# Kernel tuning notes

Measured on AMD Instinct MI355X. Metric: run time of the kernel, lower is better.

Reference implementation:

```python
import jax, jax.numpy as jnp
import numpy as np


def _conv(x, w):
    # 'same'-padded NCHW conv, stride 1, no bias (matches nn.Conv2d(..., padding=k//2, bias=False))
    return jax.lax.conv_general_dilated(x, w, (1, 1), 'SAME',
                                        dimension_numbers=('NCHW', 'OIHW', 'NCHW'))


def setup_inputs() -> dict:
    key = jax.random.key(0)
    ks = jax.random.split(key, 11)
    b, C, H, W = 8, 64, 192, 192
    n_classes, n_space = 2, 8
    return {
        'x': jax.random.normal(ks[0], (b, C, H, W), jnp.float32),
        'class_score': jax.random.normal(ks[1], (b, n_classes, H, W), jnp.float32),
        # to_cspace: Conv2d(1, n_space-1, 3, padding=1)
        'W_cspace': jax.random.normal(ks[2], (n_space - 1, 1, 3, 3), jnp.float32) * 0.1,
        # to_xspace: Conv2d(C, C*n_space, 3, padding=1)
        'W_xspace': jax.random.normal(ks[3], (C * n_space, C, 3, 3), jnp.float32) * 0.02,
        # 1x1 convs stored as squeezed vectors (no bias)
        'W_combine_space': jax.random.normal(ks[4], (n_space,), jnp.float32) * 0.3,  # Conv2d(n_space,1,1)
        'W_cvalue': jax.random.normal(ks[5], (n_space,), jnp.float32) * 0.3,        # Conv2d(1,n_space,1)
        'W_attn': jax.random.normal(ks[6], (n_space,), jnp.float32) * 0.3,          # Conv2d(1,n_space,1)
        'W_combine': jax.random.normal(ks[7], (n_space,), jnp.float32) * 0.3,       # Conv2d(n_space,1,1)
        # single_conv: Conv2d(C,C,3) + BatchNorm2d(C) + ReLU
        'W_single': jax.random.normal(ks[8], (C, C, 3, 3), jnp.float32) * 0.02,
        'bn_gamma': jnp.ones((C,), jnp.float32),
        'bn_beta': jnp.zeros((C,), jnp.float32),
    }


def reference(x, class_score, W_cspace, W_xspace, W_combine_space, W_cvalue,
              W_attn, W_combine, W_single, bn_gamma, bn_beta):
    b, C, H, Wd = x.shape
    nc = class_score.shape[1]           # n_classes
    s = W_cvalue.shape[0]               # n_space
    class_prob = jax.nn.sigmoid(class_score)                       # (b, c, H, W)

    # per-class spatial 'spaces'
    space0 = class_prob.reshape(b * nc, 1, H, Wd)                  # (b*c, 1, H, W)
    space = jnp.concatenate([space0, jax.nn.sigmoid(_conv(space0, W_cspace))], axis=1)  # (b*c, s, H, W)
    space_norm = space / jnp.sum(space, axis=(2, 3), keepdims=True)
    space_norm = space_norm.reshape(b, nc, s, H, Wd).transpose(0, 2, 1, 3, 4)  # (b, s, c, H, W)

    # project x into s spaces, then contract over spatial dims (replaces broadcast-mul + double sum)
    xv = _conv(x, W_xspace).reshape(b, s, C, H, Wd)                # (b, s, d, H, W)
    tok = jnp.einsum('bsdhw,bschw->bscd', xv, space_norm)          # (b, s, c, d)
    tok = jnp.einsum('s,bscd->bcd', W_combine_space, tok)          # combine_space 1x1 conv -> (b, c, d)

    # class value / attention (1x1 convs over a singleton channel == broadcast scale)
    cval = tok[:, None] * W_cvalue[None, :, None, None]            # (b, s, c, d)
    attn = class_prob.reshape(b, nc, H * Wd).transpose(0, 2, 1)    # (b, hw, c)
    attn = jax.nn.sigmoid(attn[:, None] * W_attn[None, :, None, None])  # (b, s, hw, c)

    # attention matmul + combine 1x1 conv fused into one contraction (linear ops commute)
    info = jnp.einsum('s,bsnc,bscd->bnd', W_combine, attn, cval)   # (b, hw, d)
    info = info.transpose(0, 2, 1).reshape(b, C, H, Wd)            # (b, d, H, W)

    # single_conv: conv3x3 -> BatchNorm2d (training-mode batch stats, biased var) -> ReLU
    y = _conv(info, W_single)
    mean = jnp.mean(y, axis=(0, 2, 3), keepdims=True)
    var = jnp.var(y, axis=(0, 2, 3), keepdims=True)
    y = jax.nn.relu((y - mean) * jax.lax.rsqrt(var + 1e-5)
                    * bn_gamma[None, :, None, None] + bn_beta[None, :, None, None])
    return x + y
```

## Files before the change

### kernel.cpp

```cpp
#include <hip/hip_runtime.h>
#include <math.h>

#define B   8
#define C   64
#define HH  192
#define WWD 192
#define P   (HH*WWD)
#define NC  2
#define NS  8
#define PP  (194*194)

#define OFF_SPACE 0
#define OFF_WT    0
#define OFF_GM    294912
#define OFF_WST   884736
#define OFF_SPART 4817408
#define OFF_R     4835840
#define OFF_TOK2  4909568
#define OFF_U     4910592
#define OFF_STP   4919808
#define OFF_SCALE 4956672
#define OFF_SHIFT 4956736
#define WS_FLOATS 4956800

__device__ __forceinline__ float sigm(float x) { return 1.0f / (1.0f + expf(-x)); }

__global__ void k_space(const float* __restrict__ cs, const float* __restrict__ Wc,
                        float* __restrict__ spp, float* __restrict__ Spart) {
    int m = blockIdx.y;
    int bx = blockIdx.x;
    int p = bx * 256 + threadIdx.x;
    int h = p / WWD, w = p - (p / WWD) * WWD;
    float cp[9];
    #pragma unroll
    for (int ky = 0; ky < 3; ky++)
        #pragma unroll
        for (int kx = 0; kx < 3; kx++) {
            int hh = h + ky - 1, ww = w + kx - 1;
            float v = 0.f;
            if ((unsigned)hh < HH && (unsigned)ww < WWD)
                v = sigm(cs[m * P + hh * WWD + ww]);
            cp[ky * 3 + kx] = v;
        }
    float ch[8];
    ch[0] = cp[4];
    #pragma unroll
    for (int j = 0; j < 7; j++) {
        float a = 0.f;
        #pragma unroll
        for (int k = 0; k < 9; k++) a += Wc[j * 9 + k] * cp[k];
        ch[j + 1] = sigm(a);
    }
    #pragma unroll
    for (int q = 0; q < 8; q++)
        spp[(m * 8 + q) * PP + (h + 1) * 194 + (w + 1)] = ch[q];
    __shared__ float red[4][8];
    int lane = threadIdx.x & 63, wave = threadIdx.x >> 6;
    #pragma unroll
    for (int q = 0; q < 8; q++) {
        float v = ch[q];
        for (int off = 32; off > 0; off >>= 1) v += __shfl_down(v, off);
        if (lane == 0) red[wave][q] = v;
    }
    __syncthreads();
    if (threadIdx.x < 8) {
        int q = threadIdx.x;
        Spart[(m * 8 + q) * 144 + bx] = red[0][q] + red[1][q] + red[2][q] + red[3][q];
    }
}

__launch_bounds__(256, 3)
__global__ void k_R2(const float* __restrict__ x, const float* __restrict__ spp,
                     float* __restrict__ R) {
    int ig = blockIdx.x;
    int scz = blockIdx.y;
    int b  = blockIdx.z;
    int sc = scz & 15;
    int half = scz >> 4;
    int s = sc >> 1, c = sc & 1;
    const float* xb = x + (b * C + ig * 8) * P;
    const float* sp = spp + ((b * NC + c) * NS + s) * PP;

    float acc[8][9];
    #pragma unroll
    for (int i = 0; i < 8; i++)
        #pragma unroll
        for (int t = 0; t < 9; t++) acc[i][t] = 0.f;

    for (int it = half * 18; it < half * 18 + 18; it++) {
        int p0 = it * 1024 + threadIdx.x * 4;
        int h = p0 / WWD, w0 = p0 - (p0 / WWD) * WWD;
        float4 xv[8];
        #pragma unroll
        for (int i = 0; i < 8; i++) xv[i] = *(const float4*)(xb + i * P + p0);
        float g[3][6];
        #pragma unroll
        for (int ty = 0; ty < 3; ty++) {
            const float* rp = sp + (h + 2 - ty) * 194 + w0;
            float4 ga; float2 gb;
            __builtin_memcpy(&ga, rp, 16);
            __builtin_memcpy(&gb, rp + 4, 8);
            g[ty][0] = ga.x; g[ty][1] = ga.y; g[ty][2] = ga.z;
            g[ty][3] = ga.w; g[ty][4] = gb.x; g[ty][5] = gb.y;
        }
        #pragma unroll
        for (int ty = 0; ty < 3; ty++)
            #pragma unroll
            for (int tx = 0; tx < 3; tx++) {
                float g0 = g[ty][2 - tx], g1 = g[ty][3 - tx];
                float g2 = g[ty][4 - tx], g3 = g[ty][5 - tx];
                #pragma unroll
                for (int i = 0; i < 8; i++) {
                    float a = acc[i][ty * 3 + tx];
                    a += xv[i].x * g0; a += xv[i].y * g1;
                    a += xv[i].z * g2; a += xv[i].w * g3;
                    acc[i][ty * 3 + tx] = a;
                }
            }
    }

    __shared__ float red[4][72];
    int lane = threadIdx.x & 63, wave = threadIdx.x >> 6;
    #pragma unroll
    for (int i = 0; i < 8; i++)
        #pragma unroll
        for (int t = 0; t < 9; t++) {
            float v = acc[i][t];
            for (int off = 32; off > 0; off >>= 1) v += __shfl_down(v, off);
            if (lane == 0) red[wave][i * 9 + t] = v;
        }
    __syncthreads();
    if (threadIdx.x < 72) {
        int i = threadIdx.x / 9, t = threadIdx.x - (threadIdx.x / 9) * 9;
        float v = red[0][threadIdx.x] + red[1][threadIdx.x] +
                  red[2][threadIdx.x] + red[3][threadIdx.x];
        atomicAdd(&R[((b * 16 + sc) * 64 + (ig * 8 + i)) * 9 + t], v);
    }
}

__global__ void k_wtb(const float* __restrict__ Wxs, const float* __restrict__ Ws,
                      float* __restrict__ Wt, float* __restrict__ WsT) {
    int blk = blockIdx.x;
    if (blk < 1152) {
        int o = blk * 256 + threadIdx.x;
        int d = o & 63, r = o >> 6;
        int s = r / 576, t = r - s * 576;
        Wt[o] = Wxs[(s * 64 + d) * 576 + t];
    } else {
        int o = (blk - 1152) * 256 + threadIdx.x;
        int ci = o / 576, q = o - ci * 576;
        int t = q >> 6, oc = q & 63;
        WsT[o] = Ws[(oc * 64 + ci) * 9 + t];
    }
}

__global__ void k_g(const float* __restrict__ cs, const float* __restrict__ Wcval,
                    const float* __restrict__ Wattn, const float* __restrict__ Wcomb,
                    float* __restrict__ gmap) {
    int m = blockIdx.y;
    int p = blockIdx.x * 256 + threadIdx.x;
    float wa[8], wt[8];
    #pragma unroll
    for (int s = 0; s < 8; s++) { wa[s] = Wcomb[s] * Wcval[s]; wt[s] = Wattn[s]; }
    float cp = sigm(cs[m * P + p]);
    float a = 0.f;
    #pragma unroll
    for (int s = 0; s < 8; s++) a += wa[s] * sigm(cp * wt[s]);
    gmap[m * P + p] = a;
}

__global__ void k_tok2(const float* __restrict__ Wt, const float* __restrict__ Wcs,
                       const float* __restrict__ R, const float* __restrict__ Spart,
                       float* __restrict__ tok2) {
    int bc = blockIdx.x, s = blockIdx.y, tz = blockIdx.z;
    int d = threadIdx.x;
    const float* spp = Spart + (bc * 8 + s) * 144;
    float sv = 0.f;
    for (int k = d; k < 144; k += 64) sv += spp[k];
    #pragma unroll
    for (int msk = 32; msk >= 1; msk >>= 1) sv += __shfl_xor(sv, msk);

    const float* Rp = R + ((bc & 1) + ((bc >> 1) * 16 + s * 2)) * 576;
    const float* Wp = Wt + s * 576 * 64 + d;
    float a = 0.f;
    int t0 = tz * 144;
    #pragma unroll 8
    for (int t = t0; t < t0 + 144; t++) a += Wp[t * 64] * Rp[t];
    float val = a * Wcs[s] / sv;
    atomicAdd(&tok2[bc * C + d], val);
}

__global__ void k_U(const float* __restrict__ WsT, const float* __restrict__ tok2,
                    float* __restrict__ U) {
    int b = blockIdx.x, m = blockIdx.y;
    int tid = threadIdx.x;
    int oc = tid & 63, t = tid >> 6;
    __shared__ float tok[64];
    if (tid < 64) tok[tid] = tok2[(b * NC + m) * C + tid];
    __syncthreads();
    float a = 0.f;
    #pragma unroll 8
    for (int ci = 0; ci < C; ci++) a += WsT[ci * 576 + tid] * tok[ci];
    U[((b * C + oc) * 2 + m) * 9 + t] = a;
}

__device__ __forceinline__ void stage_g(const float* __restrict__ gmap, int b, int ty0, int tx0,
                                        float* h0, float* h1) {
    const float* g0p = gmap + (b * NC + 0) * P;
    const float* g1p = gmap + (b * NC + 1) * P;
    for (int idx = threadIdx.x; idx < 34 * 34; idx += 256) {
        int i = idx / 34, j = idx - (idx / 34) * 34;
        int gy = ty0 - 1 + i, gx = tx0 - 1 + j;
        float a0 = 0.f, a1 = 0.f;
        if ((unsigned)gy < HH && (unsigned)gx < WWD) {
            int p = gy * WWD + gx;
            a0 = g0p[p]; a1 = g1p[p];
        }
        h0[i * 35 + j] = a0; h1[i * 35 + j] = a1;
    }
}

__launch_bounds__(256)
__global__ void k_cs(const float* __restrict__ gmap, const float* __restrict__ U,
                     float* __restrict__ STp) {
    int tile = blockIdx.x, og2 = blockIdx.y, b = blockIdx.z;
    int ty0 = (tile / 6) * 32, tx0 = (tile % 6) * 32;
    __shared__ float h0[34 * 35], h1[34 * 35];
    stage_g(gmap, b, ty0, tx0, h0, h1);
    __syncthreads();

    int w = __builtin_amdgcn_readfirstlane(threadIdx.x >> 6);
    int lane = threadIdx.x & 63;
    for (int g4 = 0; g4 < 4; g4++) {
        int oc0 = (og2 * 4 + g4) * 8 + w * 2;
        float u0[2][9], u1[2][9];
        #pragma unroll
        for (int j = 0; j < 2; j++) {
            const float* up = U + ((b * C + oc0 + j) * 2) * 9;
            #pragma unroll
            for (int t = 0; t < 9; t++) { u0[j][t] = up[t]; u1[j][t] = up[9 + t]; }
        }
        float s1[2] = {0.f, 0.f}, s2[2] = {0.f, 0.f};
        for (int it = 0; it < 4; it++) {
            int row = it * 8 + (lane >> 3);
            int c0 = (lane & 7) * 4;
            float g0v[3][6], g1v[3][6];
            #pragma unroll
            for (int dy = 0; dy < 3; dy++)
                #pragma unroll
                for (int dx = 0; dx < 6; dx++) {
                    g0v[dy][dx] = h0[(row + dy) * 35 + c0 + dx];
                    g1v[dy][dx] = h1[(row + dy) * 35 + c0 + dx];
                }
            #pragma unroll
            for (int j = 0; j < 2; j++)
                #pragma unroll
                for (int px = 0; px < 4; px++) {
                    float y = 0.f;
                    #pragma unroll
                    for (int ky = 0; ky < 3; ky++)
                        #pragma unroll
                        for (int kx = 0; kx < 3; kx++) {
                            y += u0[j][ky * 3 + kx] * g0v[ky][px + kx];
                            y += u1[j][ky * 3 + kx] * g1v[ky][px + kx];
                        }
                    s1[j] += y; s2[j] += y * y;
                }
        }
        #pragma unroll
        for (int j = 0; j < 2; j++) {
            float a = s1[j], q = s2[j];
            for (int off = 32; off > 0; off >>= 1) { a += __shfl_down(a, off); q += __shfl_down(q, off); }
            if (lane == 0) {
                int slot = b * 36 + tile;
                STp[slot * 64 + (oc0 + j)] = a;
                STp[288 * 64 + slot * 64 + (oc0 + j)] = q;
            }
        }
    }
}

__global__ void k_bnfin(const float* __restrict__ STp, const float* __restrict__ gamma,
                        const float* __restrict__ beta, float* __restrict__ scale,
                        float* __restrict__ shift) {
    int oc = threadIdx.x & 63, q = threadIdx.x >> 6;
    double s = 0.0, s2 = 0.0;
    for (int k = q * 72; k < q * 72 + 72; k++) {
        s  += (double)STp[k * 64 + oc];
        s2 += (double)STp[288 * 64 + k * 64 + oc];
    }
    __shared__ double ls[4][64], ls2[4][64];
    ls[q][oc] = s; ls2[q][oc] = s2;
    __syncthreads();
    if (threadIdx.x < 64) {
        double S  = ls[0][oc] + ls[1][oc] + ls[2][oc] + ls[3][oc];
        double S2 = ls2[0][oc] + ls2[1][oc] + ls2[2][oc] + ls2[3][oc];
        double n = (double)(B * P);
        double mean = S / n;
        double var = S2 / n - mean * mean;
        float sc = gamma[oc] * rsqrtf((float)var + 1e-5f);
        scale[oc] = sc;
        shift[oc] = beta[oc] - (float)mean * sc;
    }
}

__launch_bounds__(256)
__global__ void k_fin2(const float* __restrict__ gmap, const float* __restrict__ U,
                       const float* __restrict__ x,
                       const float* __restrict__ scale, const float* __restrict__ shift,
                       float* __restrict__ out) {
    int tile = blockIdx.x, og2 = blockIdx.y, b = blockIdx.z;
    int ty0 = (tile / 6) * 32, tx0 = (tile % 6) * 32;
    __shared__ float h0[34 * 35], h1[34 * 35];
    stage_g(gmap, b, ty0, tx0, h0, h1);
    __syncthreads();

    int w = __builtin_amdgcn_readfirstlane(threadIdx.x >> 6);
    int lane = threadIdx.x & 63;
    for (int g4 = 0; g4 < 4; g4++) {
        int oc0 = (og2 * 4 + g4) * 8 + w * 2;
        float u0[2][9], u1[2][9], sc[2], sh[2];
        #pragma unroll
        for (int j = 0; j < 2; j++) {
            const float* up = U + ((b * C + oc0 + j) * 2) * 9;
            #pragma unroll
            for (int t = 0; t < 9; t++) { u0[j][t] = up[t]; u1[j][t] = up[9 + t]; }
            sc[j] = scale[oc0 + j]; sh[j] = shift[oc0 + j];
        }
        for (int it = 0; it < 4; it++) {
            int row = it * 8 + (lane >> 3);
            int c0 = (lane & 7) * 4;
            float g0v[3][6], g1v[3][6];
            #pragma unroll
            for (int dy = 0; dy < 3; dy++)
                #pragma unroll
                for (int dx = 0; dx < 6; dx++) {
                    g0v[dy][dx] = h0[(row + dy) * 35 + c0 + dx];
                    g1v[dy][dx] = h1[(row + dy) * 35 + c0 + dx];
                }
            #pragma unroll
            for (int j = 0; j < 2; j++) {
                float y4[4];
                #pragma unroll
                for (int px = 0; px < 4; px++) {
                    float y = 0.f;
                    #pragma unroll
                    for (int ky = 0; ky < 3; ky++)
                        #pragma unroll
                        for (int kx = 0; kx < 3; kx++) {
                            y += u0[j][ky * 3 + kx] * g0v[ky][px + kx];
                            y += u1[j][ky * 3 + kx] * g1v[ky][px + kx];
                        }
                    y4[px] = y;
                }
                int ga = (b * C + oc0 + j) * P + (ty0 + row) * WWD + tx0 + c0;
                float4 xv = *(const float4*)(x + ga);
                float4 ov;
                ov.x = fmaxf(y4[0] * sc[j] + sh[j], 0.f) + xv.x;
                ov.y = fmaxf(y4[1] * sc[j] + sh[j], 0.f) + xv.y;
                ov.z = fmaxf(y4[2] * sc[j] + sh[j], 0.f) + xv.z;
                ov.w = fmaxf(y4[3] * sc[j] + sh[j], 0.f) + xv.w;
                *(float4*)(out + ga) = ov;
            }
        }
    }
}

extern "C" void kernel_launch(void* const* d_in, const int* in_sizes, int n_in,
                              void* d_out, int out_size, void* d_ws, size_t ws_size,
                              hipStream_t stream) {
    const float* x     = (const float*)d_in[0];
    const float* cs    = (const float*)d_in[1];
    const float* Wc    = (const float*)d_in[2];
    const float* Wxs   = (const float*)d_in[3];
    const float* Wcsp  = (const float*)d_in[4];
    const float* Wcval = (const float*)d_in[5];
    const float* Wattn = (const float*)d_in[6];
    const float* Wcomb = (const float*)d_in[7];
    const float* Wsing = (const float*)d_in[8];
    const float* gamma = (const float*)d_in[9];
    const float* beta  = (const float*)d_in[10];
    float* ws  = (float*)d_ws;
    float* out = (float*)d_out;

    float* spp   = ws + OFF_SPACE;
    float* Wt    = ws + OFF_WT;
    float* gmap  = ws + OFF_GM;
    float* WsT   = ws + OFF_WST;
    float* Spart = ws + OFF_SPART;
    float* R     = ws + OFF_R;
    float* tok2  = ws + OFF_TOK2;
    float* U     = ws + OFF_U;
    float* STp   = ws + OFF_STP;
    float* scale = ws + OFF_SCALE;
    float* shift = ws + OFF_SHIFT;

    hipMemsetAsync(ws, 0, (size_t)(OFF_TOK2 + 1024) * sizeof(float), stream);

    k_space<<<dim3(144, 16), 256, 0, stream>>>(cs, Wc, spp, Spart);
    k_R2   <<<dim3(8, 32, 8), 256, 0, stream>>>(x, spp, R);
    k_wtb  <<<dim3(1296), 256, 0, stream>>>(Wxs, Wsing, Wt, WsT);
    k_g    <<<dim3(144, 16), 256, 0, stream>>>(cs, Wcval, Wattn, Wcomb, gmap);
    k_tok2 <<<dim3(16, 8, 4), 64, 0, stream>>>(Wt, Wcsp, R, Spart, tok2);
    k_U    <<<dim3(8, 2), 576, 0, stream>>>(WsT, tok2, U);
    k_cs   <<<dim3(36, 2, 8), 256, 0, stream>>>(gmap, U, STp);
    k_bnfin<<<1, 256, 0, stream>>>(STp, gamma, beta, scale, shift);
    k_fin2 <<<dim3(36, 2, 8), 256, 0, stream>>>(gmap, U, x, scale, shift, out);
}
```

Baseline: 380.2 us.

## Compute spatial correlation R with split-bf16 MFMA over LDS-staged space maps

Rewrites k_R2 so that the x-by-shifted-space correlation runs on MFMA bf16 16x16x32 instructions instead of scalar FMAs. Each fp32 operand is split into a high and a low bf16 part, and three products are summed to approximate fp32 accuracy. Space maps for a two-row band are staged in LDS as hi/lo bf16 planes, and each block covers all 16 space/class maps and all 64 channels. The grid changes to 96x8 blocks with direct atomicAdds from accumulators. This reduces ALU work and x re-reads, at the cost of a small precision loss and more atomics per element.

```diff
diff --git a/kernel.cpp b/kernel.cpp
--- a/kernel.cpp
+++ b/kernel.cpp
@@ -23,6 +23,9 @@
 #define OFF_SHIFT 4956736
 #define WS_FLOATS 4956800
 
+typedef __attribute__((ext_vector_type(8))) short bfrag;
+typedef __attribute__((ext_vector_type(4))) float ffrag;
+
 __device__ __forceinline__ float sigm(float x) { return 1.0f / (1.0f + expf(-x)); }
 
 __global__ void k_space(const float* __restrict__ cs, const float* __restrict__ Wc,
@@ -69,73 +72,116 @@
     }
 }
 
+#define GH_MAP 804
+#define GH_ROW 200
+
+__device__ __forceinline__ void bfpair(float v0, float v1, unsigned& h, unsigned& lo) {
+    unsigned u0 = __float_as_uint(v0), u1 = __float_as_uint(v1);
+    float r0 = v0 - __uint_as_float(u0 & 0xffff0000u);
+    float r1 = v1 - __uint_as_float(u1 & 0xffff0000u);
+    h  = (u0 >> 16) | (u1 & 0xffff0000u);
+    lo = (__float_as_uint(r0) >> 16) | (__float_as_uint(r1) & 0xffff0000u);
+}
+
+__device__ __forceinline__ bfrag mkfrag(unsigned a, unsigned b, unsigned c, unsigned d) {
+    unsigned q[4] = {a, b, c, d};
+    bfrag f;
+    __builtin_memcpy(&f, q, 16);
+    return f;
+}
+
 __launch_bounds__(256, 3)
 __global__ void k_R2(const float* __restrict__ x, const float* __restrict__ spp,
                      float* __restrict__ R) {
-    int ig = blockIdx.x;
-    int scz = blockIdx.y;
-    int b  = blockIdx.z;
-    int sc = scz & 15;
-    int half = scz >> 4;
-    int s = sc >> 1, c = sc & 1;
-    const float* xb = x + (b * C + ig * 8) * P;
-    const float* sp = spp + ((b * NC + c) * NS + s) * PP;
-
-    float acc[8][9];
-    #pragma unroll
-    for (int i = 0; i < 8; i++)
-        #pragma unroll
-        for (int t = 0; t < 9; t++) acc[i][t] = 0.f;
-
-    for (int it = half * 18; it < half * 18 + 18; it++) {
-        int p0 = it * 1024 + threadIdx.x * 4;
-        int h = p0 / WWD, w0 = p0 - (p0 / WWD) * WWD;
-        float4 xv[8];
-        #pragma unroll
-        for (int i = 0; i < 8; i++) xv[i] = *(const float4*)(xb + i * P + p0);
-        float g[3][6];
-        #pragma unroll
-        for (int ty = 0; ty < 3; ty++) {
-            const float* rp = sp + (h + 2 - ty) * 194 + w0;
-            float4 ga; float2 gb;
-            __builtin_memcpy(&ga, rp, 16);
-            __builtin_memcpy(&gb, rp + 4, 8);
-            g[ty][0] = ga.x; g[ty][1] = ga.y; g[ty][2] = ga.z;
-            g[ty][3] = ga.w; g[ty][4] = gb.x; g[ty][5] = gb.y;
-        }
-        #pragma unroll
-        for (int ty = 0; ty < 3; ty++)
-            #pragma unroll
-            for (int tx = 0; tx < 3; tx++) {
-                float g0 = g[ty][2 - tx], g1 = g[ty][3 - tx];
-                float g2 = g[ty][4 - tx], g3 = g[ty][5 - tx];
-                #pragma unroll
-                for (int i = 0; i < 8; i++) {
-                    float a = acc[i][ty * 3 + tx];
-                    a += xv[i].x * g0; a += xv[i].y * g1;
-                    a += xv[i].z * g2; a += xv[i].w * g3;
-                    acc[i][ty * 3 + tx] = a;
-                }
+    int hc = blockIdx.x;
+    int b  = blockIdx.y;
+    int tid = threadIdx.x;
+    int wv = tid >> 6, l = tid & 63;
+    int h0 = hc * 2;
+
+    __shared__ unsigned short gh[16 * GH_MAP], gl[16 * GH_MAP];
+
+    for (int idx = tid; idx < 16 * 4 * 194; idx += 256) {
+        int n = idx / 776;
+        int rem = idx - n * 776;
+        int r = rem / 194, col = rem - r * 194;
+        const float* sp = spp + ((b * NC + (n & 1)) * NS + (n >> 1)) * PP;
+        float v = sp[(h0 + r) * 194 + col];
+        unsigned u = __float_as_uint(v);
+        float res = v - __uint_as_float(u & 0xffff0000u);
+        gh[n * GH_MAP + r * GH_ROW + col] = (unsigned short)(u >> 16);
+        gl[n * GH_MAP + r * GH_ROW + col] = (unsigned short)(__float_as_uint(res) >> 16);
+    }
+    __syncthreads();
+
+    ffrag acc[3][3];
+    #pragma unroll
+    for (int a = 0; a < 3; a++)
+        #pragma unroll
+        for (int d = 0; d < 3; d++) acc[a][d] = (ffrag){0.f, 0.f, 0.f, 0.f};
+
+    int i0 = wv * 16;
+    int g8 = (l >> 4) * 8;
+    const float* xbase = x + (size_t)((b * C + i0 + (l & 15)) * HH) * WWD;
+    const unsigned short* ghn = gh + (l & 15) * GH_MAP + g8;
+    const unsigned short* gln = gl + (l & 15) * GH_MAP + g8;
+
+    for (int lr = 0; lr < 2; lr++) {
+        const float* xr = xbase + (h0 + lr) * WWD + g8;
+        #pragma unroll
+        for (int ks = 0; ks < 6; ks++) {
+            float4 a0 = *(const float4*)(xr + ks * 32);
+            float4 a1 = *(const float4*)(xr + ks * 32 + 4);
+            unsigned ah0, ah1, ah2, ah3, al0, al1, al2, al3;
+            bfpair(a0.x, a0.y, ah0, al0);
+            bfpair(a0.z, a0.w, ah1, al1);
+            bfpair(a1.x, a1.y, ah2, al2);
+            bfpair(a1.z, a1.w, ah3, al3);
+            bfrag ah = mkfrag(ah0, ah1, ah2, ah3);
+            bfrag al = mkfrag(al0, al1, al2, al3);
+            #pragma unroll
+            for (int dy = 0; dy < 3; dy++) {
+                const unsigned short* ph = ghn + (lr + dy) * GH_ROW + ks * 32;
+                const unsigned short* pl = gln + (lr + dy) * GH_ROW + ks * 32;
+                unsigned uh[5], ul[5];
+                *(uint2*)&uh[0] = *(const uint2*)(ph);
+                *(uint2*)&uh[2] = *(const uint2*)(ph + 4);
+                uh[4] = *(const unsigned*)(ph + 8);
+                *(uint2*)&ul[0] = *(const uint2*)(pl);
+                *(uint2*)&ul[2] = *(const uint2*)(pl + 4);
+                ul[4] = *(const unsigned*)(pl + 8);
+                bfrag bh0 = mkfrag(uh[0], uh[1], uh[2], uh[3]);
+                bfrag bh1 = mkfrag((uh[0] >> 16) | (uh[1] << 16), (uh[1] >> 16) | (uh[2] << 16),
+                                   (uh[2] >> 16) | (uh[3] << 16), (uh[3] >> 16) | (uh[4] << 16));
+                bfrag bh2 = mkfrag(uh[1], uh[2], uh[3], uh[4]);
+                bfrag bl0 = mkfrag(ul[0], ul[1], ul[2], ul[3]);
+                bfrag bl1 = mkfrag((ul[0] >> 16) | (ul[1] << 16), (ul[1] >> 16) | (ul[2] << 16),
+                                   (ul[2] >> 16) | (ul[3] << 16), (ul[3] >> 16) | (ul[4] << 16));
+                bfrag bl2 = mkfrag(ul[1], ul[2], ul[3], ul[4]);
+                acc[dy][0] = __builtin_amdgcn_mfma_f32_16x16x32_bf16(ah, bh0, acc[dy][0], 0, 0, 0);
+                acc[dy][0] = __builtin_amdgcn_mfma_f32_16x16x32_bf16(ah, bl0, acc[dy][0], 0, 0, 0);
+                acc[dy][0] = __builtin_amdgcn_mfma_f32_16x16x32_bf16(al, bh0, acc[dy][0], 0, 0, 0);
+                acc[dy][1] = __builtin_amdgcn_mfma_f32_16x16x32_bf16(ah, bh1, acc[dy][1], 0, 0, 0);
+                acc[dy][1] = __builtin_amdgcn_mfma_f32_16x16x32_bf16(ah, bl1, acc[dy][1], 0, 0, 0);
+                acc[dy][1] = __builtin_amdgcn_mfma_f32_16x16x32_bf16(al, bh1, acc[dy][1], 0, 0, 0);
+                acc[dy][2] = __builtin_amdgcn_mfma_f32_16x16x32_bf16(ah, bh2, acc[dy][2], 0, 0, 0);
+                acc[dy][2] = __builtin_amdgcn_mfma_f32_16x16x32_bf16(ah, bl2, acc[dy][2], 0, 0, 0);
+                acc[dy][2] = __builtin_amdgcn_mfma_f32_16x16x32_bf16(al, bh2, acc[dy][2], 0, 0, 0);
             }
-    }
-
-    __shared__ float red[4][72];
-    int lane = threadIdx.x & 63, wave = threadIdx.x >> 6;
-    #pragma unroll
-    for (int i = 0; i < 8; i++)
-        #pragma unroll
-        for (int t = 0; t < 9; t++) {
-            float v = acc[i][t];
-            for (int off = 32; off > 0; off >>= 1) v += __shfl_down(v, off);
-            if (lane == 0) red[wave][i * 9 + t] = v;
-        }
-    __syncthreads();
-    if (threadIdx.x < 72) {
-        int i = threadIdx.x / 9, t = threadIdx.x - (threadIdx.x / 9) * 9;
-        float v = red[0][threadIdx.x] + red[1][threadIdx.x] +
-                  red[2][threadIdx.x] + red[3][threadIdx.x];
-        atomicAdd(&R[((b * 16 + sc) * 64 + (ig * 8 + i)) * 9 + t], v);
-    }
+        }
+    }
+
+    #pragma unroll
+    for (int dy = 0; dy < 3; dy++)
+        #pragma unroll
+        for (int dx = 0; dx < 3; dx++) {
+            int t = 8 - (dy * 3 + dx);
+            #pragma unroll
+            for (int rg = 0; rg < 4; rg++) {
+                int i = i0 + (l >> 4) * 4 + rg;
+                atomicAdd(&R[((b * 16 + (l & 15)) * 64 + i) * 9 + t], acc[dy][dx][rg]);
+            }
+        }
 }
 
 __global__ void k_wtb(const float* __restrict__ Wxs, const float* __restrict__ Ws,
@@ -398,7 +444,7 @@
     hipMemsetAsync(ws, 0, (size_t)(OFF_TOK2 + 1024) * sizeof(float), stream);
 
     k_space<<<dim3(144, 16), 256, 0, stream>>>(cs, Wc, spp, Spart);
-    k_R2   <<<dim3(8, 32, 8), 256, 0, stream>>>(x, spp, R);
+    k_R2   <<<dim3(96, 8), 256, 0, stream>>>(x, spp, R);
     k_wtb  <<<dim3(1296), 256, 0, stream>>>(Wxs, Wsing, Wt, WsT);
     k_g    <<<dim3(144, 16), 256, 0, stream>>>(cs, Wcval, Wattn, Wcomb, gmap);
     k_tok2 <<<dim3(16, 8, 4), 64, 0, stream>>>(Wt, Wcsp, R, Spart, tok2);
```

After: 663.6 us. 1.75x slower.
